# Kernel tuning notes

Measured on AMD Instinct MI355X. Metric: run time of the kernel, lower is better.

## Reference

```python
import jax, jax.numpy as jnp
from jax import lax
import numpy as np

STEP = 0.1            # step_size
INC = 1.5             # bracket_expansion_increase
MAX_EXPAND = 16       # fixed cap on bracket-expansion iterations (masked no-ops after convergence)
MAX_SHRINK = 24       # fixed cap on shrinkage-rejection iterations


def setup_inputs() -> dict:
    key = jax.random.key(0)
    kx, kw = jax.random.split(key)
    B, D = 65536, 128
    x = jax.random.normal(kx, (B, D), jnp.float32)
    W = jax.random.normal(kw, (D, D), jnp.float32) / np.float32(np.sqrt(D))
    return {"x": x, "W": W}


def _potential(x, W):
    # correlated Gaussian potential: -0.5 * ||W x||^2, per chain
    z = x @ W.T                      # [B, D]
    return -0.5 * jnp.sum(z * z, axis=-1)  # [B]


def _slice_sample(x, W):
    B = x.shape[0]
    key = jax.random.key(42)
    k_y, k_dir, k_u0, k_shr = jax.random.split(key, 4)

    pot = _potential(x, W)                               # [B]
    # y = log(1 - u) + potential  (log of uniform height under the density)
    y = jnp.log1p(-jax.random.uniform(k_y, pot.shape, jnp.float32)) + pot

    dirs = jax.random.normal(k_dir, x.shape, jnp.float32)
    dirs = dirs / jnp.linalg.norm(dirs, axis=-1, keepdims=True)  # unit slice directions

    mask0 = y < pot

    # --- bracket expansion (lower: sign=-1, upper: sign=+1), masked fixed-trip scan ---
    def expand(sign):
        def body(carry, i):
            b, mask = carry
            step_i = STEP * jnp.power(jnp.float32(INC), i.astype(jnp.float32))
            b = jnp.where(mask, b + sign * step_i, b)
            pot_b = _potential(x + b[:, None] * dirs, W)
            mask = mask & (y < pot_b)
            return (b, mask), None
        (b, _), _ = lax.scan(body, (jnp.zeros((B,), jnp.float32), mask0),
                             jnp.arange(MAX_EXPAND))
        return b

    lb = expand(-1.0)
    ub = expand(+1.0)

    # --- initial proposal on the bracket ---
    u = jax.random.uniform(k_u0, (B,), jnp.float32) * (ub - lb) + lb
    x_new = x + u[:, None] * dirs
    mask = _potential(x_new, W) < y   # rejected chains

    # --- shrinkage loop (masked fixed-trip scan) ---
    def shrink(carry, k):
        u, lb, ub, x_new, mask = carry
        smaller = u < 0
        lb = jnp.where(mask & smaller, u, lb)
        ub = jnp.where(mask & ~smaller, u, ub)
        u_prop = jax.random.uniform(k, (B,), jnp.float32) * (ub - lb) + lb
        u = jnp.where(mask, u_prop, u)
        cand = x + u[:, None] * dirs
        pot_c = _potential(cand, W)
        x_new = jnp.where(mask[:, None], cand, x_new)
        mask = mask & (pot_c < y)
        return (u, lb, ub, x_new, mask), None

    keys = jax.random.split(k_shr, MAX_SHRINK)
    (u, lb, ub, x_new, mask), _ = lax.scan(shrink, (u, lb, ub, x_new, mask), keys)
    return x_new


def reference(x, W):
    return _slice_sample(x, W)
```

## Files before the change

### kernel.cpp

```cpp
#include <hip/hip_runtime.h>
#include <stdint.h>
#include <math.h>


#define BD 128
#define NB 65536
#define WS 132

__host__ __device__ inline uint32_t rotl32(uint32_t v, int s) {
  return (v << s) | (v >> (32 - s));
}

__host__ __device__ inline void tf2x32(uint32_t k0, uint32_t k1,
                                       uint32_t c0, uint32_t c1,
                                       uint32_t* o0, uint32_t* o1) {
  uint32_t ks2 = k0 ^ k1 ^ 0x1BD11BDAu;
  uint32_t x0 = c0 + k0, x1 = c1 + k1;
#define TFR(r) x0 += x1; x1 = rotl32(x1, (r)); x1 ^= x0;
  TFR(13) TFR(15) TFR(26) TFR(6)
  x0 += k1;  x1 += ks2 + 1u;
  TFR(17) TFR(29) TFR(16) TFR(24)
  x0 += ks2; x1 += k0 + 2u;
  TFR(13) TFR(15) TFR(26) TFR(6)
  x0 += k0;  x1 += k1 + 3u;
  TFR(17) TFR(29) TFR(16) TFR(24)
  x0 += k1;  x1 += ks2 + 4u;
  TFR(13) TFR(15) TFR(26) TFR(6)
  x0 += ks2; x1 += k0 + 5u;
#undef TFR
  *o0 = x0; *o1 = x1;
}

__device__ inline uint32_t jbits(uint32_t k0, uint32_t k1, uint32_t n) {
  uint32_t a, b;
  tf2x32(k0, k1, 0u, n, &a, &b);
  return a ^ b;
}

__device__ inline float u01(uint32_t bits) {
  return __fsub_rn(__uint_as_float((bits >> 9) | 0x3f800000u), 1.0f);
}

__device__ inline float xla_log1p(float x) {
  float u  = __fadd_rn(x, 1.0f);
  float lg = (float)log((double)u);
  float sm = __fmul_rn(__fadd_rn(__fmul_rn(-0.5f, x), 1.0f), x);
  return (fabsf(x) < 1e-4f) ? sm : lg;
}

__device__ inline float xla_erfinv(float x) {
  float xx = __fmul_rn(x, x);
  float w  = -xla_log1p(-xx);
  float p;
  if (w < 5.0f) {
    float ww = __fsub_rn(w, 2.5f);
    p = 2.81022636e-08f;
    p = __fadd_rn(3.43273939e-07f,  __fmul_rn(p, ww));
    p = __fadd_rn(-3.5233877e-06f,  __fmul_rn(p, ww));
    p = __fadd_rn(-4.39150654e-06f, __fmul_rn(p, ww));
    p = __fadd_rn(0.00021858087f,   __fmul_rn(p, ww));
    p = __fadd_rn(-0.00125372503f,  __fmul_rn(p, ww));
    p = __fadd_rn(-0.00417768164f,  __fmul_rn(p, ww));
    p = __fadd_rn(0.246640727f,     __fmul_rn(p, ww));
    p = __fadd_rn(1.50140941f,      __fmul_rn(p, ww));
  } else {
    float ww = __fsub_rn(__fsqrt_rn(w), 3.0f);
    p = -0.000200214257f;
    p = __fadd_rn(0.000100950558f,  __fmul_rn(p, ww));
    p = __fadd_rn(0.00134934322f,   __fmul_rn(p, ww));
    p = __fadd_rn(-0.00367342844f,  __fmul_rn(p, ww));
    p = __fadd_rn(0.00573950773f,   __fmul_rn(p, ww));
    p = __fadd_rn(-0.0076224613f,   __fmul_rn(p, ww));
    p = __fadd_rn(0.00943887047f,   __fmul_rn(p, ww));
    p = __fadd_rn(1.00167406f,      __fmul_rn(p, ww));
    p = __fadd_rn(2.83297682f,      __fmul_rn(p, ww));
  }
  return __fmul_rn(p, x);
}

__device__ __attribute__((always_inline)) inline float potential16(
    const float* __restrict__ xr, const float* __restrict__ dr,
    const float* __restrict__ wr, float coef) {
  float z[8] = {0.f, 0.f, 0.f, 0.f, 0.f, 0.f, 0.f, 0.f};
#pragma unroll 2
  for (int q = 0; q < 32; ++q) {
    float4 xv = *(const float4*)(xr + q * 4);
    float4 dv = *(const float4*)(dr + q * 4);
    float c0 = __fadd_rn(xv.x, __fmul_rn(coef, dv.x));
    float c1 = __fadd_rn(xv.y, __fmul_rn(coef, dv.y));
    float c2 = __fadd_rn(xv.z, __fmul_rn(coef, dv.z));
    float c3 = __fadd_rn(xv.w, __fmul_rn(coef, dv.w));
#pragma unroll
    for (int m = 0; m < 8; ++m) {
      float4 wv = *(const float4*)(wr + m * (16 * WS) + q * 4);
      z[m] = __fmaf_rn(c0, wv.x, z[m]);
      z[m] = __fmaf_rn(c1, wv.y, z[m]);
      z[m] = __fmaf_rn(c2, wv.z, z[m]);
      z[m] = __fmaf_rn(c3, wv.w, z[m]);
    }
  }
  float pr = 0.0f;
#pragma unroll
  for (int m = 0; m < 8; ++m) pr = __fadd_rn(pr, __fmul_rn(z[m], z[m]));
#pragma unroll
  for (int msk = 32; msk >= 4; msk >>= 1)
    pr = __fadd_rn(pr, __shfl_xor(pr, msk));
  return __fmul_rn(-0.5f, pr);
}

__device__ inline double epsb(float u) {
  double au = fabs((double)u);
  return 1.5e-3 + 2e-4 * au + 2e-5 * au * au;
}

struct KeyArgs {
  uint32_t ky0, ky1;
  uint32_t ku0, ku1;
  uint32_t kd0, kd1;
  uint32_t ks[48];
};

__global__ __launch_bounds__(1024, 1) void slice_fused_kernel(
    const float* __restrict__ X, const float* __restrict__ Wg,
    float* __restrict__ OUT, KeyArgs ka) {
  __shared__ __align__(16) float Wl[128 * WS];
  __shared__ __align__(16) float Xl[64 * WS];
  __shared__ __align__(16) float Dl[64 * WS];

  const int tid   = threadIdx.x;
  const int cbase = blockIdx.x * 64;

  for (int i = tid; i < 128 * 32; i += 1024) {
    int r = i >> 5, q = i & 31;
    *(float4*)&Wl[r * WS + q * 4] = ((const float4*)Wg)[i];
  }
  for (int i = tid; i < 64 * 32; i += 1024) {
    int c = i >> 5, q = i & 31;
    *(float4*)&Xl[c * WS + q * 4] = ((const float4*)(X + (size_t)(cbase + c) * BD))[q];
  }

  const int wave = tid >> 6, lane = tid & 63;
  const int c    = lane & 3;
  const int j    = lane >> 2;
  const int cl   = wave * 4 + c;
  const uint32_t chain = (uint32_t)(cbase + cl);

  {
    const float LO    = __uint_as_float(0xBF7FFFFFu);
    const float SQRT2 = __uint_as_float(0x3FB504F3u);
    float vm[8];
#pragma unroll
    for (int m = 0; m < 8; ++m) {
      uint32_t n = chain * 128u + (uint32_t)(16 * m + j);
      float f  = u01(jbits(ka.kd0, ka.kd1, n));
      float um = fmaxf(LO, __fadd_rn(__fmul_rn(f, 2.0f), LO));
      vm[m] = __fmul_rn(SQRT2, xla_erfinv(um));
    }
    float pr = 0.0f;
#pragma unroll
    for (int m = 0; m < 8; ++m) pr = __fadd_rn(pr, __fmul_rn(vm[m], vm[m]));
#pragma unroll
    for (int msk = 32; msk >= 4; msk >>= 1)
      pr = __fadd_rn(pr, __shfl_xor(pr, msk));
    float nrm = __fsqrt_rn(pr);
#pragma unroll
    for (int m = 0; m < 8; ++m)
      Dl[cl * WS + 16 * m + j] = vm[m] / nrm;
  }

  __syncthreads();

  const float* xr = &Xl[cl * WS];
  const float* dr = &Dl[cl * WS];
  const float* wr = &Wl[j * WS];

  float za[8], zb[8];
#pragma unroll
  for (int m = 0; m < 8; ++m) { za[m] = 0.0f; zb[m] = 0.0f; }
#pragma unroll 2
  for (int q = 0; q < 32; ++q) {
    float4 xv = *(const float4*)(xr + q * 4);
    float4 dv = *(const float4*)(dr + q * 4);
#pragma unroll
    for (int m = 0; m < 8; ++m) {
      float4 wv = *(const float4*)(wr + m * (16 * WS) + q * 4);
      za[m] = __fmaf_rn(xv.x, wv.x, za[m]);
      za[m] = __fmaf_rn(xv.y, wv.y, za[m]);
      za[m] = __fmaf_rn(xv.z, wv.z, za[m]);
      za[m] = __fmaf_rn(xv.w, wv.w, za[m]);
      zb[m] = __fmaf_rn(dv.x, wv.x, zb[m]);
      zb[m] = __fmaf_rn(dv.y, wv.y, zb[m]);
      zb[m] = __fmaf_rn(dv.z, wv.z, zb[m]);
      zb[m] = __fmaf_rn(dv.w, wv.w, zb[m]);
    }
  }

  float pr0 = 0.0f;
#pragma unroll
  for (int m = 0; m < 8; ++m) pr0 = __fadd_rn(pr0, __fmul_rn(za[m], za[m]));
#pragma unroll
  for (int msk = 32; msk >= 4; msk >>= 1)
    pr0 = __fadd_rn(pr0, __shfl_xor(pr0, msk));
  float pot0 = __fmul_rn(-0.5f, pr0);

  double gl = 0.0, hl = 0.0;
#pragma unroll
  for (int m = 0; m < 8; ++m) {
    gl += (double)za[m] * (double)zb[m];
    hl += (double)zb[m] * (double)zb[m];
  }
#pragma unroll
  for (int msk = 32; msk >= 4; msk >>= 1) {
    gl += __shfl_xor(gl, msk);
    hl += __shfl_xor(hl, msk);
  }
  const double g = gl, h = hl;
  const double potd0 = (double)pot0;

  float Uy = u01(jbits(ka.ky0, ka.ky1, chain));
  float y  = __fadd_rn(xla_log1p(-Uy), pot0);
  const double yd = (double)y;
  bool mask0 = (y < pot0);

  float lb = 0.0f, ub = 0.0f;
#pragma unroll 1
  for (int side = 0; side < 2; ++side) {
    bool m = mask0;
    float b = 0.0f, pw = 1.0f;
#pragma unroll 1
    for (int i = 0; i < 16; ++i) {
      if (!__any((int)m)) break;
      float step = __fmul_rn(0.1f, pw);
      pw = __fmul_rn(pw, 1.5f);
      if (m) b = side ? __fadd_rn(b, step) : __fsub_rn(b, step);
      double bd   = (double)b;
      double diff = (potd0 - bd * g - 0.5 * bd * bd * h) - yd;
      bool need = m && (fabs(diff) <= epsb(b));
      float pe = 0.0f;
      if (__any((int)need)) pe = potential16(xr, dr, wr, b);
      bool cont = need ? (y < pe) : (diff > 0.0);
      m = m && cont;
    }
    if (side == 0) lb = b; else ub = b;
  }

  float U0 = u01(jbits(ka.ku0, ka.ku1, chain));
  float u  = __fadd_rn(__fmul_rn(U0, __fsub_rn(ub, lb)), lb);
  bool rej;
  {
    double ud   = (double)u;
    double diff = (potd0 - ud * g - 0.5 * ud * ud * h) - yd;
    bool need = fabs(diff) <= epsb(u);
    float pe = 0.0f;
    if (__any((int)need)) pe = potential16(xr, dr, wr, u);
    rej = need ? (pe < y) : (diff < 0.0);
  }

#pragma unroll 1
  for (int t = 0; t < 24; ++t) {
    if (!__any((int)rej)) break;
    if (rej) {
      if (u < 0.0f) lb = u; else ub = u;
      float Ut = u01(jbits(ka.ks[2 * t], ka.ks[2 * t + 1], chain));
      u = __fadd_rn(__fmul_rn(Ut, __fsub_rn(ub, lb)), lb);
    }
    double ud   = (double)u;
    double diff = (potd0 - ud * g - 0.5 * ud * ud * h) - yd;
    bool need = rej && (fabs(diff) <= epsb(u));
    float pe = 0.0f;
    if (__any((int)need)) pe = potential16(xr, dr, wr, u);
    bool rj = need ? (pe < y) : (diff < 0.0);
    rej = rej && rj;
  }

  float* orow = OUT + (size_t)chain * BD;
#pragma unroll
  for (int hh = 0; hh < 2; ++hh) {
    int q = j * 2 + hh;
    float4 xv = *(const float4*)(xr + q * 4);
    float4 dv = *(const float4*)(dr + q * 4);
    float4 o;
    o.x = __fadd_rn(xv.x, __fmul_rn(u, dv.x));
    o.y = __fadd_rn(xv.y, __fmul_rn(u, dv.y));
    o.z = __fadd_rn(xv.z, __fmul_rn(u, dv.z));
    o.w = __fadd_rn(xv.w, __fmul_rn(u, dv.w));
    *(float4*)&orow[q * 4] = o;
  }
}

extern "C" void kernel_launch(void* const* d_in, const int* in_sizes, int n_in,
                              void* d_out, int out_size, void* d_ws, size_t ws_size,
                              hipStream_t stream) {
  (void)in_sizes; (void)n_in; (void)d_ws; (void)ws_size; (void)out_size;
  const float* x = (const float*)d_in[0];
  const float* W = (const float*)d_in[1];
  float* out = (float*)d_out;

  const uint32_t R0 = 0u, R1 = 42u;
  uint32_t ky0, ky1, kd0, kd1, ku0, ku1, ksh0, ksh1;
  tf2x32(R0, R1, 0u, 0u, &ky0, &ky1);
  tf2x32(R0, R1, 0u, 1u, &kd0, &kd1);
  tf2x32(R0, R1, 0u, 2u, &ku0, &ku1);
  tf2x32(R0, R1, 0u, 3u, &ksh0, &ksh1);

  KeyArgs ka;
  ka.ky0 = ky0; ka.ky1 = ky1; ka.ku0 = ku0; ka.ku1 = ku1;
  ka.kd0 = kd0; ka.kd1 = kd1;
  for (uint32_t t = 0; t < 24; ++t) {
    uint32_t a, b;
    tf2x32(ksh0, ksh1, 0u, t, &a, &b);
    ka.ks[2 * t] = a; ka.ks[2 * t + 1] = b;
  }

  slice_fused_kernel<<<dim3(NB / 64), dim3(1024), 0, stream>>>(x, W, out, ka);
}
```

Baseline: 157.0 us.

## Read W from global/L2 in packed layout, shrink blocks for occupancy, tighten epsilon

Drops the 66KB shared-memory copy of W and reads W straight from global memory (L2-cached). When workspace is available, a small pre-kernel repacks W first so each lane's float4 reads are coalesced. Blocks shrink to 32 chains and 512 threads with launch bounds asking for 6 blocks per CU, to raise occupancy now that LDS use is much smaller. The quadratic-approximation error bound is also tightened so fewer chains need the exact potential, which risks wrong accept/reject decisions if the bound is too tight.

```diff
diff --git a/kernel.cpp b/kernel.cpp
--- a/kernel.cpp
+++ b/kernel.cpp
@@ -6,6 +6,8 @@
 #define BD 128
 #define NB 65536
 #define WS 132
+#define CPB 32
+#define TPB 512
 
 __host__ __device__ inline uint32_t rotl32(uint32_t v, int s) {
   return (v << s) | (v >> (32 - s));
@@ -78,9 +80,17 @@
   return __fmul_rn(p, x);
 }
 
+__global__ __launch_bounds__(1024) void pack_w_kernel(
+    const float* __restrict__ Wg, float* __restrict__ Wp) {
+  int i = blockIdx.x * 1024 + threadIdx.x;
+  int e = i & 3, j = (i >> 2) & 15, m = (i >> 6) & 7, q = i >> 9;
+  Wp[i] = Wg[(16 * m + j) * 128 + q * 4 + e];
+}
+
+template <bool PACKED>
 __device__ __attribute__((always_inline)) inline float potential16(
     const float* __restrict__ xr, const float* __restrict__ dr,
-    const float* __restrict__ wr, float coef) {
+    const float* __restrict__ Wsrc, int j, float coef) {
   float z[8] = {0.f, 0.f, 0.f, 0.f, 0.f, 0.f, 0.f, 0.f};
 #pragma unroll 2
   for (int q = 0; q < 32; ++q) {
@@ -92,7 +102,9 @@
     float c3 = __fadd_rn(xv.w, __fmul_rn(coef, dv.w));
 #pragma unroll
     for (int m = 0; m < 8; ++m) {
-      float4 wv = *(const float4*)(wr + m * (16 * WS) + q * 4);
+      const float* wa = PACKED ? (Wsrc + (((q * 8 + m) * 16 + j) << 2))
+                               : (Wsrc + (16 * m + j) * 128 + q * 4);
+      float4 wv = *(const float4*)wa;
       z[m] = __fmaf_rn(c0, wv.x, z[m]);
       z[m] = __fmaf_rn(c1, wv.y, z[m]);
       z[m] = __fmaf_rn(c2, wv.z, z[m]);
@@ -110,7 +122,7 @@
 
 __device__ inline double epsb(float u) {
   double au = fabs((double)u);
-  return 1.5e-3 + 2e-4 * au + 2e-5 * au * au;
+  return 4e-4 + 8e-5 * au + 8e-6 * au * au;
 }
 
 struct KeyArgs {
@@ -120,21 +132,17 @@
   uint32_t ks[48];
 };
 
-__global__ __launch_bounds__(1024, 1) void slice_fused_kernel(
-    const float* __restrict__ X, const float* __restrict__ Wg,
+template <bool PACKED>
+__global__ __launch_bounds__(TPB, 6) void slice_fused_kernel(
+    const float* __restrict__ X, const float* __restrict__ Wsrc,
     float* __restrict__ OUT, KeyArgs ka) {
-  __shared__ __align__(16) float Wl[128 * WS];
-  __shared__ __align__(16) float Xl[64 * WS];
-  __shared__ __align__(16) float Dl[64 * WS];
+  __shared__ __align__(16) float Xl[CPB * WS];
+  __shared__ __align__(16) float Dl[CPB * WS];
 
   const int tid   = threadIdx.x;
-  const int cbase = blockIdx.x * 64;
-
-  for (int i = tid; i < 128 * 32; i += 1024) {
-    int r = i >> 5, q = i & 31;
-    *(float4*)&Wl[r * WS + q * 4] = ((const float4*)Wg)[i];
-  }
-  for (int i = tid; i < 64 * 32; i += 1024) {
+  const int cbase = blockIdx.x * CPB;
+
+  for (int i = tid; i < CPB * 32; i += TPB) {
     int c = i >> 5, q = i & 31;
     *(float4*)&Xl[c * WS + q * 4] = ((const float4*)(X + (size_t)(cbase + c) * BD))[q];
   }
@@ -172,7 +180,6 @@
 
   const float* xr = &Xl[cl * WS];
   const float* dr = &Dl[cl * WS];
-  const float* wr = &Wl[j * WS];
 
   float za[8], zb[8];
 #pragma unroll
@@ -183,7 +190,9 @@
     float4 dv = *(const float4*)(dr + q * 4);
 #pragma unroll
     for (int m = 0; m < 8; ++m) {
-      float4 wv = *(const float4*)(wr + m * (16 * WS) + q * 4);
+      const float* wa = PACKED ? (Wsrc + (((q * 8 + m) * 16 + j) << 2))
+                               : (Wsrc + (16 * m + j) * 128 + q * 4);
+      float4 wv = *(const float4*)wa;
       za[m] = __fmaf_rn(xv.x, wv.x, za[m]);
       za[m] = __fmaf_rn(xv.y, wv.y, za[m]);
       za[m] = __fmaf_rn(xv.z, wv.z, za[m]);
@@ -237,7 +246,7 @@
       double diff = (potd0 - bd * g - 0.5 * bd * bd * h) - yd;
       bool need = m && (fabs(diff) <= epsb(b));
       float pe = 0.0f;
-      if (__any((int)need)) pe = potential16(xr, dr, wr, b);
+      if (__any((int)need)) pe = potential16<PACKED>(xr, dr, Wsrc, j, b);
       bool cont = need ? (y < pe) : (diff > 0.0);
       m = m && cont;
     }
@@ -252,7 +261,7 @@
     double diff = (potd0 - ud * g - 0.5 * ud * ud * h) - yd;
     bool need = fabs(diff) <= epsb(u);
     float pe = 0.0f;
-    if (__any((int)need)) pe = potential16(xr, dr, wr, u);
+    if (__any((int)need)) pe = potential16<PACKED>(xr, dr, Wsrc, j, u);
     rej = need ? (pe < y) : (diff < 0.0);
   }
 
@@ -268,7 +277,7 @@
     double diff = (potd0 - ud * g - 0.5 * ud * ud * h) - yd;
     bool need = rej && (fabs(diff) <= epsb(u));
     float pe = 0.0f;
-    if (__any((int)need)) pe = potential16(xr, dr, wr, u);
+    if (__any((int)need)) pe = potential16<PACKED>(xr, dr, Wsrc, j, u);
     bool rj = need ? (pe < y) : (diff < 0.0);
     rej = rej && rj;
   }
@@ -291,7 +300,7 @@
 extern "C" void kernel_launch(void* const* d_in, const int* in_sizes, int n_in,
                               void* d_out, int out_size, void* d_ws, size_t ws_size,
                               hipStream_t stream) {
-  (void)in_sizes; (void)n_in; (void)d_ws; (void)ws_size; (void)out_size;
+  (void)in_sizes; (void)n_in; (void)out_size;
   const float* x = (const float*)d_in[0];
   const float* W = (const float*)d_in[1];
   float* out = (float*)d_out;
@@ -312,5 +321,13 @@
     ka.ks[2 * t] = a; ka.ks[2 * t + 1] = b;
   }
 
-  slice_fused_kernel<<<dim3(NB / 64), dim3(1024), 0, stream>>>(x, W, out, ka);
-}
+  const bool packed = (ws_size >= (size_t)(BD * BD * sizeof(float)));
+  if (packed) {
+    pack_w_kernel<<<dim3(16), dim3(1024), 0, stream>>>(W, (float*)d_ws);
+    slice_fused_kernel<true><<<dim3(NB / CPB), dim3(TPB), 0, stream>>>(
+        x, (const float*)d_ws, out, ka);
+  } else {
+    slice_fused_kernel<false><<<dim3(NB / CPB), dim3(TPB), 0, stream>>>(
+        x, W, out, ka);
+  }
+}
```

Result: slower. 177.5 us (+13.1%).
